# Performance work log

Measured on AMD Instinct MI355X. Metric: run time of the kernel, lower is better.

## Reference

```python
import jax, jax.numpy as jnp
import numpy as np

B, T, D, H = 2, 2048, 768, 12
HS = D // H           # head_size = 64
FF = 4 * D            # feed_forward_multiplier = 4 -> hidden 3072
HALF = FF // 2        # SwiGLU halves hidden -> 1536
EPS = 1e-8


def rmsnorm(x, scale):
    # RMSNorm with p=-1: full-dim L2 norm / sqrt(d), then x/(rms+eps)*scale
    d = x.shape[-1]
    rms = jnp.linalg.norm(x, axis=-1, keepdims=True) * (d ** -0.5)
    return scale * (x / (rms + EPS))


def setup_inputs() -> dict:
    key = jax.random.key(0)
    ks = jax.random.split(key, 12)
    s = 0.02
    return {
        "x":  jax.random.normal(ks[0], (B, T, D), dtype=jnp.float32),
        "Wq": jax.random.normal(ks[1], (H, D, HS), dtype=jnp.float32) * s,
        "Wk": jax.random.normal(ks[2], (H, D, HS), dtype=jnp.float32) * s,
        "Wv": jax.random.normal(ks[3], (H, D, HS), dtype=jnp.float32) * s,
        "Wo": jax.random.normal(ks[4], (D, D), dtype=jnp.float32) * s,
        "bo": jnp.zeros((D,), dtype=jnp.float32),
        "W1": jax.random.normal(ks[5], (D, FF), dtype=jnp.float32) * s,
        "b1": jnp.zeros((FF,), dtype=jnp.float32),
        "W2": jax.random.normal(ks[6], (HALF, D), dtype=jnp.float32) * s,
        "b2": jnp.zeros((D,), dtype=jnp.float32),
        "g1": jnp.ones((D,), dtype=jnp.float32),
        "g2": jnp.ones((D,), dtype=jnp.float32),
    }


def reference(x, Wq, Wk, Wv, Wo, bo, W1, b1, W2, b2, g1, g2):
    Bx, Tx, Dx = x.shape
    # --- Multi-head causal attention (pre-RMSNorm, residual) ---
    h = rmsnorm(x, g1)
    q = jnp.einsum('btd,hdk->bhtk', h, Wq)
    k = jnp.einsum('btd,hdk->bhtk', h, Wk)
    v = jnp.einsum('btd,hdk->bhtk', h, Wv)
    # NOTE: original scales by C**-0.5 where C = embed_dim (not head_size)
    scores = jnp.einsum('bhtk,bhsk->bhts', q, k) * (Dx ** -0.5)
    causal = jnp.tril(jnp.ones((Tx, Tx), dtype=bool))
    scores = jnp.where(causal, scores, -jnp.inf)
    wei = jax.nn.softmax(scores, axis=-1)
    attn = jnp.einsum('bhts,bhsk->bhtk', wei, v)
    attn = attn.transpose(0, 2, 1, 3).reshape(Bx, Tx, Dx)  # concat heads
    x = x + attn @ Wo + bo
    # --- SwiGLU FFN (pre-RMSNorm, residual) ---
    h2 = rmsnorm(x, g2)
    u = h2 @ W1 + b1
    a, gate = jnp.split(u, 2, axis=-1)  # chunk: first half = value, second = gate
    x = x + (jax.nn.silu(gate) * a) @ W2 + b2
    return x
```

## Files before the change

### kernel.cpp

```cpp
#include <hip/hip_runtime.h>
#include <math.h>

#define TDIM 2048
#define DDIM 768
#define NH   12
#define NROWS 4096
#define EPSV 1e-8f
#define SCALE 0.03608439182435161f

typedef __bf16 bf16_t;
typedef bf16_t bf16x8 __attribute__((ext_vector_type(8)));
typedef bf16_t bf16x4 __attribute__((ext_vector_type(4)));
typedef float  floatx4 __attribute__((ext_vector_type(4)));

__device__ __forceinline__ void glds16(const bf16_t* g, bf16_t* l) {
    __builtin_amdgcn_global_load_lds(
        (const __attribute__((address_space(1))) void*)g,
        (__attribute__((address_space(3))) void*)l, 16, 0, 0);
}

__global__ __launch_bounds__(256) void pack_all(
    const float* __restrict__ Wq, const float* __restrict__ Wk,
    const float* __restrict__ Wv, const float* __restrict__ Wo,
    const float* __restrict__ W1, const float* __restrict__ W2,
    bf16_t* __restrict__ qkvw, bf16_t* __restrict__ wo,
    bf16_t* __restrict__ w1, bf16_t* __restrict__ w2)
{
    int bid = blockIdx.x;
    const float* src; bf16_t* dst;
    int srcld, dstld, k0, n0;
    if (bid < 144) {
        int kx = bid % 12, nx = bid / 12;
        src = Wo; dst = wo; srcld = 768; dstld = 768; k0 = kx * 64; n0 = nx * 64;
    } else if (bid < 720) {
        int t = bid - 144; int kx = t % 12, nx = t / 12;
        src = W1; dst = w1; srcld = 3072; dstld = 768; k0 = kx * 64; n0 = nx * 64;
    } else if (bid < 1008) {
        int t = bid - 720; int kx = t % 24, nx = t / 24;
        src = W2; dst = w2; srcld = 768; dstld = 1536; k0 = kx * 64; n0 = nx * 64;
    } else {
        int t = bid - 1008; int kx = t % 12, y = t / 12;
        int sel = y / 12, h = y - sel * 12;
        src = ((sel == 0) ? Wq : (sel == 1) ? Wk : Wv) + (size_t)h * 768 * 64;
        dst = qkvw + (size_t)(sel * 768 + h * 64) * 768;
        srcld = 64; dstld = 768; k0 = kx * 64; n0 = 0;
    }
    __shared__ float Ts[64][65];
    int tid = threadIdx.x;
    int r = tid >> 2, c = (tid & 3) * 16;
    const float* s = src + (size_t)(k0 + r) * srcld + n0 + c;
    #pragma unroll
    for (int i = 0; i < 4; i++) {
        float4 t = *(const float4*)(s + i * 4);
        Ts[r][c + i*4 + 0] = t.x; Ts[r][c + i*4 + 1] = t.y;
        Ts[r][c + i*4 + 2] = t.z; Ts[r][c + i*4 + 3] = t.w;
    }
    __syncthreads();
    int n = tid >> 2, kk = (tid & 3) * 16;
    bf16x8 o0, o1;
    #pragma unroll
    for (int i = 0; i < 8; i++) {
        o0[i] = (bf16_t)Ts[kk + i][n];
        o1[i] = (bf16_t)Ts[kk + 8 + i][n];
    }
    bf16_t* d = dst + (size_t)(n0 + n) * dstld + k0 + kk;
    *(bf16x8*)d = o0;
    *(bf16x8*)(d + 8) = o1;
}

__global__ __launch_bounds__(256) void rmsnorm_bf(
    const float* __restrict__ x, const float* __restrict__ g,
    bf16_t* __restrict__ out)
{
    int row = blockIdx.x;
    int tid = threadIdx.x;
    const float* xr = x + (size_t)row * DDIM;
    float v0 = xr[tid], v1 = xr[tid + 256], v2 = xr[tid + 512];
    float s = v0*v0 + v1*v1 + v2*v2;
    #pragma unroll
    for (int off = 32; off > 0; off >>= 1)
        s += __shfl_down(s, off, 64);
    __shared__ float red[4];
    __shared__ float tot;
    if ((tid & 63) == 0) red[tid >> 6] = s;
    __syncthreads();
    if (tid == 0) tot = red[0] + red[1] + red[2] + red[3];
    __syncthreads();
    float rms = sqrtf(tot * (1.0f / DDIM));
    float inv = 1.0f / (rms + EPSV);
    bf16_t* orow = out + (size_t)row * DDIM;
    orow[tid]       = (bf16_t)(g[tid]       * v0 * inv);
    orow[tid + 256] = (bf16_t)(g[tid + 256] * v1 * inv);
    orow[tid + 512] = (bf16_t)(g[tid + 512] * v2 * inv);
}

template<int TM>
__global__ __launch_bounds__(256) void gemm_bf16(
    const bf16_t* __restrict__ A, const bf16_t* __restrict__ BT, int K,
    float* __restrict__ Cf, bf16_t* __restrict__ Cb, int ldc,
    const float* __restrict__ bias, const float* __restrict__ resid)
{
    constexpr int MT = TM / 32;
    __shared__ bf16_t As0[TM][32], As1[TM][32];
    __shared__ bf16_t Bs0[128][32], Bs1[128][32];
    int tid = threadIdx.x;
    int wave = tid >> 6, lane = tid & 63;
    int lrow = lane & 15, quad = lane >> 4;
    int wm = wave >> 1, wn = wave & 1;

    int m0 = blockIdx.y * TM;
    int n0 = blockIdx.x * 128;

    int srow = lane >> 2, scol = (lane & 3) * 8;
    const bf16_t* Ag = A  + ((size_t)m0 + wave * (TM/4) + srow) * K + scol;
    const bf16_t* Bg = BT + ((size_t)n0 + wave * 32 + srow) * K + scol;

    floatx4 acc[MT][4];
    #pragma unroll
    for (int mt = 0; mt < MT; mt++)
        #pragma unroll
        for (int nt = 0; nt < 4; nt++)
            #pragma unroll
            for (int r = 0; r < 4; r++) acc[mt][nt][r] = 0.f;

    for (int k0 = 0; k0 < K; k0 += 64) {
        __syncthreads();
        #pragma unroll
        for (int i = 0; i < TM/64; i++) {
            glds16(Ag + (size_t)(i*16) * K + k0,      &As0[wave*(TM/4) + i*16][0]);
            glds16(Ag + (size_t)(i*16) * K + k0 + 32, &As1[wave*(TM/4) + i*16][0]);
        }
        #pragma unroll
        for (int i = 0; i < 2; i++) {
            glds16(Bg + (size_t)(i*16) * K + k0,      &Bs0[wave*32 + i*16][0]);
            glds16(Bg + (size_t)(i*16) * K + k0 + 32, &Bs1[wave*32 + i*16][0]);
        }
        __syncthreads();

        bf16x8 af0[MT], af1[MT], bf0[4], bf1[4];
        #pragma unroll
        for (int mt = 0; mt < MT; mt++) {
            af0[mt] = *(const bf16x8*)&As0[wm*(TM/2) + mt*16 + lrow][quad * 8];
            af1[mt] = *(const bf16x8*)&As1[wm*(TM/2) + mt*16 + lrow][quad * 8];
        }
        #pragma unroll
        for (int nt = 0; nt < 4; nt++) {
            bf0[nt] = *(const bf16x8*)&Bs0[wn*64 + nt*16 + lrow][quad * 8];
            bf1[nt] = *(const bf16x8*)&Bs1[wn*64 + nt*16 + lrow][quad * 8];
        }
        #pragma unroll
        for (int mt = 0; mt < MT; mt++)
            #pragma unroll
            for (int nt = 0; nt < 4; nt++) {
                acc[mt][nt] = __builtin_amdgcn_mfma_f32_16x16x32_bf16(
                    bf0[nt], af0[mt], acc[mt][nt], 0, 0, 0);
                acc[mt][nt] = __builtin_amdgcn_mfma_f32_16x16x32_bf16(
                    bf1[nt], af1[mt], acc[mt][nt], 0, 0, 0);
            }
    }

    int crow0 = m0 + wm * (TM/2);
    int ccol0 = n0 + wn * 64;
    #pragma unroll
    for (int mt = 0; mt < MT; mt++) {
        int row = crow0 + mt * 16 + lrow;
        #pragma unroll
        for (int nt = 0; nt < 4; nt++) {
            int col = ccol0 + nt * 16 + quad * 4;
            size_t off = (size_t)row * ldc + col;
            float4 bv = make_float4(0.f, 0.f, 0.f, 0.f);
            if (bias) bv = *(const float4*)(bias + col);
            float4 rs = make_float4(0.f, 0.f, 0.f, 0.f);
            if (resid) rs = *(const float4*)(resid + off);
            floatx4 a = acc[mt][nt];
            if (Cf) {
                float4 v;
                v.x = a[0] + bv.x + rs.x; v.y = a[1] + bv.y + rs.y;
                v.z = a[2] + bv.z + rs.z; v.w = a[3] + bv.w + rs.w;
                *(float4*)(Cf + off) = v;
            } else {
                bf16x4 v;
                v[0] = (bf16_t)(a[0] + bv.x + rs.x);
                v[1] = (bf16_t)(a[1] + bv.y + rs.y);
                v[2] = (bf16_t)(a[2] + bv.z + rs.z);
                v[3] = (bf16_t)(a[3] + bv.w + rs.w);
                *(bf16x4*)(Cb + off) = v;
            }
        }
    }
}

__global__ __launch_bounds__(256) void vt_kernel(
    const bf16_t* __restrict__ qkv, bf16_t* __restrict__ vt)
{
    __shared__ bf16_t Ts[64][72];
    int t0 = blockIdx.x * 64;
    int bh = blockIdx.y;
    int b = bh / NH, h = bh - b * NH;
    int tid = threadIdx.x;
    int r = tid >> 2, c = (tid & 3) * 16;
    const bf16_t* src = qkv + ((size_t)b * TDIM + t0 + r) * 2304 + 1536 + h * 64 + c;
    *(bf16x8*)&Ts[r][c]     = *(const bf16x8*)src;
    *(bf16x8*)&Ts[r][c + 8] = *(const bf16x8*)(src + 8);
    __syncthreads();
    int d = tid >> 2, tt = (tid & 3) * 16;
    bf16x8 o0, o1;
    #pragma unroll
    for (int i = 0; i < 8; i++) {
        o0[i] = Ts[tt + i][d];
        o1[i] = Ts[tt + 8 + i][d];
    }
    bf16_t* dst = vt + ((size_t)bh * 64 + d) * TDIM + t0 + tt;
    *(bf16x8*)dst = o0;
    *(bf16x8*)(dst + 8) = o1;
}

__global__ __launch_bounds__(256) void attn_mfma(
    const bf16_t* __restrict__ qkv, const bf16_t* __restrict__ vt,
    bf16_t* __restrict__ o)
{
    const int QS = 2304;
    int bid = blockIdx.x;
    int j = bid & 255, slot = bid >> 8;
    int qt, bh;
    if (slot == 0)      { qt = j & 31;        bh = j >> 5; }
    else if (slot == 1) { qt = 31 - (j & 31); bh = 8 + (j >> 5); }
    else                { qt = j >> 3;        bh = 16 + (j & 7); }
    int b = bh / NH, h = bh - b * NH;
    int tid = threadIdx.x;
    int wave = tid >> 6, lane = tid & 63;
    int lrow = lane & 15, quad = lane >> 4;

    __shared__ bf16_t Ks[64][72];
    __shared__ bf16_t Vt[64][72];
    __shared__ bf16_t Ps[4][16][72];

    size_t rbase = (size_t)b * TDIM;
    int q0 = qt * 64, qrow_w = q0 + wave * 16;

    const bf16_t* qp = qkv + (rbase + qrow_w + lrow) * QS + h * 64;
    bf16x8 qf[2];
    qf[0] = *(const bf16x8*)(qp + quad * 8);
    qf[1] = *(const bf16x8*)(qp + 32 + quad * 8);

    floatx4 o_acc[4];
    #pragma unroll
    for (int mt = 0; mt < 4; mt++)
        #pragma unroll
        for (int r = 0; r < 4; r++) o_acc[mt][r] = 0.f;
    float m_r = -INFINITY, l_r = 0.f;

    int srow = tid >> 2;
    int scol = (tid & 3) * 16;

    for (int s = 0; s <= qt; s++) {
        __syncthreads();
        {
            const bf16_t* kp = qkv + (rbase + s * 64 + srow) * QS + 768 + h * 64 + scol;
            *(bf16x8*)&Ks[srow][scol]     = *(const bf16x8*)kp;
            *(bf16x8*)&Ks[srow][scol + 8] = *(const bf16x8*)(kp + 8);
            const bf16_t* vp = vt + ((size_t)bh * 64 + srow) * TDIM + s * 64 + scol;
            *(bf16x8*)&Vt[srow][scol]     = *(const bf16x8*)vp;
            *(bf16x8*)&Vt[srow][scol + 8] = *(const bf16x8*)(vp + 8);
        }
        __syncthreads();

        floatx4 sfrag[4];
        #pragma unroll
        for (int nt = 0; nt < 4; nt++) {
            floatx4 a;
            #pragma unroll
            for (int r = 0; r < 4; r++) a[r] = 0.f;
            #pragma unroll
            for (int kf = 0; kf < 2; kf++) {
                bf16x8 afr = *(const bf16x8*)&Ks[nt * 16 + lrow][kf * 32 + quad * 8];
                a = __builtin_amdgcn_mfma_f32_16x16x32_bf16(afr, qf[kf], a, 0, 0, 0);
            }
            sfrag[nt] = a;
        }

        if (s == qt) {
            int qg = qrow_w + lrow;
            #pragma unroll
            for (int nt = 0; nt < 4; nt++)
                #pragma unroll
                for (int r = 0; r < 4; r++) {
                    int kc = s * 64 + nt * 16 + quad * 4 + r;
                    sfrag[nt][r] = (kc > qg) ? -INFINITY : sfrag[nt][r] * SCALE;
                }
        } else {
            #pragma unroll
            for (int nt = 0; nt < 4; nt++)
                #pragma unroll
                for (int r = 0; r < 4; r++) sfrag[nt][r] *= SCALE;
        }

        float mx = sfrag[0][0];
        #pragma unroll
        for (int nt = 0; nt < 4; nt++)
            #pragma unroll
            for (int r = 0; r < 4; r++) mx = fmaxf(mx, sfrag[nt][r]);
        mx = fmaxf(mx, __shfl_xor(mx, 16, 64));
        mx = fmaxf(mx, __shfl_xor(mx, 32, 64));
        float mn = fmaxf(m_r, mx);
        float alpha = __expf(m_r - mn);
        m_r = mn;

        float ls = 0.f;
        #pragma unroll
        for (int nt = 0; nt < 4; nt++) {
            bf16x4 pv;
            #pragma unroll
            for (int r = 0; r < 4; r++) {
                float p = __expf(sfrag[nt][r] - mn);
                ls += p;
                pv[r] = (bf16_t)p;
            }
            *(bf16x4*)&Ps[wave][lrow][nt * 16 + quad * 4] = pv;
        }
        ls += __shfl_xor(ls, 16, 64);
        ls += __shfl_xor(ls, 32, 64);
        l_r = l_r * alpha + ls;
        #pragma unroll
        for (int mt = 0; mt < 4; mt++)
            #pragma unroll
            for (int r = 0; r < 4; r++) o_acc[mt][r] *= alpha;

        #pragma unroll
        for (int kf = 0; kf < 2; kf++) {
            bf16x8 pfr = *(const bf16x8*)&Ps[wave][lrow][kf * 32 + quad * 8];
            #pragma unroll
            for (int mt = 0; mt < 4; mt++) {
                bf16x8 vfr = *(const bf16x8*)&Vt[mt * 16 + lrow][kf * 32 + quad * 8];
                o_acc[mt] = __builtin_amdgcn_mfma_f32_16x16x32_bf16(vfr, pfr, o_acc[mt], 0, 0, 0);
            }
        }
    }

    float inv = 1.0f / l_r;
    size_t rb = (rbase + qrow_w + lrow) * DDIM + h * 64;
    #pragma unroll
    for (int mt = 0; mt < 4; mt++) {
        bf16x4 ov;
        #pragma unroll
        for (int r = 0; r < 4; r++) ov[r] = (bf16_t)(o_acc[mt][r] * inv);
        *(bf16x4*)(o + rb + mt * 16 + quad * 4) = ov;
    }
}

__global__ __launch_bounds__(192) void swiglu_bf(
    const bf16_t* __restrict__ u, bf16_t* __restrict__ sw)
{
    int row = blockIdx.x;
    int j0 = threadIdx.x * 8;
    bf16x8 a = *(const bf16x8*)(u + (size_t)row * 3072 + j0);
    bf16x8 g = *(const bf16x8*)(u + (size_t)row * 3072 + 1536 + j0);
    bf16x8 r;
    #pragma unroll
    for (int i = 0; i < 8; i++) {
        float gv = (float)g[i];
        r[i] = (bf16_t)((float)a[i] * (gv / (1.0f + __expf(-gv))));
    }
    *(bf16x8*)(sw + (size_t)row * 1536 + j0) = r;
}

extern "C" void kernel_launch(void* const* d_in, const int* in_sizes, int n_in,
                              void* d_out, int out_size, void* d_ws, size_t ws_size,
                              hipStream_t stream) {
    const float* x  = (const float*)d_in[0];
    const float* Wq = (const float*)d_in[1];
    const float* Wk = (const float*)d_in[2];
    const float* Wv = (const float*)d_in[3];
    const float* Wo = (const float*)d_in[4];
    const float* bo = (const float*)d_in[5];
    const float* W1 = (const float*)d_in[6];
    const float* b1 = (const float*)d_in[7];
    const float* W2 = (const float*)d_in[8];
    const float* b2 = (const float*)d_in[9];
    const float* g1 = (const float*)d_in[10];
    const float* g2 = (const float*)d_in[11];
    float* out = (float*)d_out;
    char* ws = (char*)d_ws;

    bf16_t* qkvw_bt = (bf16_t*)(ws);
    bf16_t* wo_bt   = (bf16_t*)(ws + 3538944);
    bf16_t* w1_bt   = (bf16_t*)(ws + 4718592);
    bf16_t* w2_bt   = (bf16_t*)(ws + 9437184);
    bf16_t* h_bf    = (bf16_t*)(ws + 11796480);
    bf16_t* qkv     = (bf16_t*)(ws + 18087936);
    bf16_t* attn_bf = (bf16_t*)(ws + 36962304);
    bf16_t* u_bf    = (bf16_t*)(ws + 43253760);
    bf16_t* sw_bf   = (bf16_t*)(ws + 68419584);
    bf16_t* vt      = (bf16_t*)(ws + 81002496);

    pack_all<<<1440, 256, 0, stream>>>(Wq, Wk, Wv, Wo, W1, W2,
                                       qkvw_bt, wo_bt, w1_bt, w2_bt);

    rmsnorm_bf<<<NROWS, 256, 0, stream>>>(x, g1, h_bf);

    gemm_bf16<128><<<dim3(18, 32), 256, 0, stream>>>(
        h_bf, qkvw_bt, 768, nullptr, qkv, 2304, nullptr, nullptr);

    vt_kernel<<<dim3(32, 24), 256, 0, stream>>>(qkv, vt);

    attn_mfma<<<768, 256, 0, stream>>>(qkv, vt, attn_bf);

    gemm_bf16<64><<<dim3(6, 64), 256, 0, stream>>>(
        attn_bf, wo_bt, 768, out, nullptr, 768, bo, x);

    rmsnorm_bf<<<NROWS, 256, 0, stream>>>(out, g2, h_bf);

    gemm_bf16<128><<<dim3(24, 32), 256, 0, stream>>>(
        h_bf, w1_bt, 768, nullptr, u_bf, 3072, b1, nullptr);

    swiglu_bf<<<NROWS, 192, 0, stream>>>(u_bf, sw_bf);

    gemm_bf16<64><<<dim3(6, 64), 256, 0, stream>>>(
        sw_bf, w2_bt, 1536, out, nullptr, 768, b2, out);
}
```

Measured before the change: 269.1 us.

## Fuse SwiGLU into W1 GEMM epilogue and double-buffer attention K/V tiles

Interleaves the value and gate columns of W1 during packing so that each GEMM lane holds matching value/gate pairs. SwiGLU can then be applied in the W1 GEMM epilogue, which removes the separate swiglu kernel and the round trip of the 3072-wide intermediate through memory. The attention kernel now double-buffers K/V tiles in LDS with register prefetch two tiles ahead, cutting one barrier per iteration. It also raises wave priority around the MFMAs and skips the online-softmax rescale unless the running max grows by more than a threshold. The lazy rescale lets exponentials reach up to e^8 before renormalising, and the interleaved bf16x2 stores are narrower than before.

```diff
diff --git a/kernel.cpp b/kernel.cpp
--- a/kernel.cpp
+++ b/kernel.cpp
@@ -11,6 +11,7 @@
 typedef __bf16 bf16_t;
 typedef bf16_t bf16x8 __attribute__((ext_vector_type(8)));
 typedef bf16_t bf16x4 __attribute__((ext_vector_type(4)));
+typedef bf16_t bf16x2 __attribute__((ext_vector_type(2)));
 typedef float  floatx4 __attribute__((ext_vector_type(4)));
 
 __device__ __forceinline__ void glds16(const bf16_t* g, bf16_t* l) {
@@ -29,12 +30,14 @@
     int bid = blockIdx.x;
     const float* src; bf16_t* dst;
     int srcld, dstld, k0, n0;
+    int remap = 0;
     if (bid < 144) {
         int kx = bid % 12, nx = bid / 12;
         src = Wo; dst = wo; srcld = 768; dstld = 768; k0 = kx * 64; n0 = nx * 64;
     } else if (bid < 720) {
         int t = bid - 144; int kx = t % 12, nx = t / 12;
         src = W1; dst = w1; srcld = 3072; dstld = 768; k0 = kx * 64; n0 = nx * 64;
+        remap = 1;
     } else if (bid < 1008) {
         int t = bid - 720; int kx = t % 24, nx = t / 24;
         src = W2; dst = w2; srcld = 768; dstld = 1536; k0 = kx * 64; n0 = nx * 64;
@@ -63,7 +66,9 @@
         o0[i] = (bf16_t)Ts[kk + i][n];
         o1[i] = (bf16_t)Ts[kk + 8 + i][n];
     }
-    bf16_t* d = dst + (size_t)(n0 + n) * dstld + k0 + kk;
+    int oc = n0 + n;
+    if (remap) oc = (oc < 1536) ? (oc * 2) : ((oc - 1536) * 2 + 1);
+    bf16_t* d = dst + (size_t)oc * dstld + k0 + kk;
     *(bf16x8*)d = o0;
     *(bf16x8*)(d + 8) = o1;
 }
@@ -94,7 +99,7 @@
     orow[tid + 512] = (bf16_t)(g[tid + 512] * v2 * inv);
 }
 
-template<int TM>
+template<int TM, int EPI>
 __global__ __launch_bounds__(256) void gemm_bf16(
     const bf16_t* __restrict__ A, const bf16_t* __restrict__ BT, int K,
     float* __restrict__ Cf, bf16_t* __restrict__ Cb, int ldc,
@@ -167,24 +172,36 @@
         #pragma unroll
         for (int nt = 0; nt < 4; nt++) {
             int col = ccol0 + nt * 16 + quad * 4;
-            size_t off = (size_t)row * ldc + col;
-            float4 bv = make_float4(0.f, 0.f, 0.f, 0.f);
-            if (bias) bv = *(const float4*)(bias + col);
-            float4 rs = make_float4(0.f, 0.f, 0.f, 0.f);
-            if (resid) rs = *(const float4*)(resid + off);
             floatx4 a = acc[mt][nt];
-            if (Cf) {
-                float4 v;
-                v.x = a[0] + bv.x + rs.x; v.y = a[1] + bv.y + rs.y;
-                v.z = a[2] + bv.z + rs.z; v.w = a[3] + bv.w + rs.w;
-                *(float4*)(Cf + off) = v;
+            if constexpr (EPI == 1) {
+                int c = col >> 1;
+                float2 ba = *(const float2*)(bias + c);
+                float2 bg = *(const float2*)(bias + 1536 + c);
+                float a0 = a[0] + ba.x, g0 = a[1] + bg.x;
+                float a1 = a[2] + ba.y, g1 = a[3] + bg.y;
+                bf16x2 v;
+                v[0] = (bf16_t)(a0 * (g0 / (1.0f + __expf(-g0))));
+                v[1] = (bf16_t)(a1 * (g1 / (1.0f + __expf(-g1))));
+                *(bf16x2*)(Cb + (size_t)row * ldc + c) = v;
             } else {
-                bf16x4 v;
-                v[0] = (bf16_t)(a[0] + bv.x + rs.x);
-                v[1] = (bf16_t)(a[1] + bv.y + rs.y);
-                v[2] = (bf16_t)(a[2] + bv.z + rs.z);
-                v[3] = (bf16_t)(a[3] + bv.w + rs.w);
-                *(bf16x4*)(Cb + off) = v;
+                size_t off = (size_t)row * ldc + col;
+                float4 bv = make_float4(0.f, 0.f, 0.f, 0.f);
+                if (bias) bv = *(const float4*)(bias + col);
+                float4 rs = make_float4(0.f, 0.f, 0.f, 0.f);
+                if (resid) rs = *(const float4*)(resid + off);
+                if (Cf) {
+                    float4 v;
+                    v.x = a[0] + bv.x + rs.x; v.y = a[1] + bv.y + rs.y;
+                    v.z = a[2] + bv.z + rs.z; v.w = a[3] + bv.w + rs.w;
+                    *(float4*)(Cf + off) = v;
+                } else {
+                    bf16x4 v;
+                    v[0] = (bf16_t)(a[0] + bv.x + rs.x);
+                    v[1] = (bf16_t)(a[1] + bv.y + rs.y);
+                    v[2] = (bf16_t)(a[2] + bv.z + rs.z);
+                    v[3] = (bf16_t)(a[3] + bv.w + rs.w);
+                    *(bf16x4*)(Cb + off) = v;
+                }
             }
         }
     }
@@ -231,8 +248,8 @@
     int wave = tid >> 6, lane = tid & 63;
     int lrow = lane & 15, quad = lane >> 4;
 
-    __shared__ bf16_t Ks[64][72];
-    __shared__ bf16_t Vt[64][72];
+    __shared__ bf16_t Ks[2][64][72];
+    __shared__ bf16_t Vts[2][64][72];
     __shared__ bf16_t Ps[4][16][72];
 
     size_t rbase = (size_t)b * TDIM;
@@ -252,20 +269,31 @@
 
     int srow = tid >> 2;
     int scol = (tid & 3) * 16;
+    const bf16_t* kbase = qkv + (rbase + srow) * QS + 768 + h * 64 + scol;
+    const bf16_t* vbase = vt + ((size_t)bh * 64 + srow) * TDIM + scol;
+
+    bf16x8 kr0 = *(const bf16x8*)kbase;
+    bf16x8 kr1 = *(const bf16x8*)(kbase + 8);
+    bf16x8 vr0 = *(const bf16x8*)vbase;
+    bf16x8 vr1 = *(const bf16x8*)(vbase + 8);
+    *(bf16x8*)&Ks[0][srow][scol]      = kr0;
+    *(bf16x8*)&Ks[0][srow][scol + 8]  = kr1;
+    *(bf16x8*)&Vts[0][srow][scol]     = vr0;
+    *(bf16x8*)&Vts[0][srow][scol + 8] = vr1;
+    if (qt >= 1) {
+        const bf16_t* kp = kbase + (size_t)64 * QS;
+        const bf16_t* vp = vbase + 64;
+        kr0 = *(const bf16x8*)kp;  kr1 = *(const bf16x8*)(kp + 8);
+        vr0 = *(const bf16x8*)vp;  vr1 = *(const bf16x8*)(vp + 8);
+    }
+    asm volatile("s_waitcnt lgkmcnt(0)" ::: "memory");
+    __builtin_amdgcn_s_barrier();
 
     for (int s = 0; s <= qt; s++) {
-        __syncthreads();
-        {
-            const bf16_t* kp = qkv + (rbase + s * 64 + srow) * QS + 768 + h * 64 + scol;
-            *(bf16x8*)&Ks[srow][scol]     = *(const bf16x8*)kp;
-            *(bf16x8*)&Ks[srow][scol + 8] = *(const bf16x8*)(kp + 8);
-            const bf16_t* vp = vt + ((size_t)bh * 64 + srow) * TDIM + s * 64 + scol;
-            *(bf16x8*)&Vt[srow][scol]     = *(const bf16x8*)vp;
-            *(bf16x8*)&Vt[srow][scol + 8] = *(const bf16x8*)(vp + 8);
-        }
-        __syncthreads();
+        int cur = s & 1;
 
         floatx4 sfrag[4];
+        __builtin_amdgcn_s_setprio(1);
         #pragma unroll
         for (int nt = 0; nt < 4; nt++) {
             floatx4 a;
@@ -273,10 +301,19 @@
             for (int r = 0; r < 4; r++) a[r] = 0.f;
             #pragma unroll
             for (int kf = 0; kf < 2; kf++) {
-                bf16x8 afr = *(const bf16x8*)&Ks[nt * 16 + lrow][kf * 32 + quad * 8];
+                bf16x8 afr = *(const bf16x8*)&Ks[cur][nt * 16 + lrow][kf * 32 + quad * 8];
                 a = __builtin_amdgcn_mfma_f32_16x16x32_bf16(afr, qf[kf], a, 0, 0, 0);
             }
             sfrag[nt] = a;
+        }
+        __builtin_amdgcn_s_setprio(0);
+
+        if (s < qt) {
+            int nxt = cur ^ 1;
+            *(bf16x8*)&Ks[nxt][srow][scol]      = kr0;
+            *(bf16x8*)&Ks[nxt][srow][scol + 8]  = kr1;
+            *(bf16x8*)&Vts[nxt][srow][scol]     = vr0;
+            *(bf16x8*)&Vts[nxt][srow][scol + 8] = vr1;
         }
 
         if (s == qt) {
@@ -302,9 +339,16 @@
             for (int r = 0; r < 4; r++) mx = fmaxf(mx, sfrag[nt][r]);
         mx = fmaxf(mx, __shfl_xor(mx, 16, 64));
         mx = fmaxf(mx, __shfl_xor(mx, 32, 64));
-        float mn = fmaxf(m_r, mx);
-        float alpha = __expf(m_r - mn);
-        m_r = mn;
+        if (__any(mx > m_r + 8.0f)) {
+            float mn = fmaxf(m_r, mx);
+            float alpha = __expf(m_r - mn);
+            m_r = mn;
+            l_r *= alpha;
+            #pragma unroll
+            for (int mt = 0; mt < 4; mt++)
+                #pragma unroll
+                for (int r = 0; r < 4; r++) o_acc[mt][r] *= alpha;
+        }
 
         float ls = 0.f;
         #pragma unroll
@@ -312,7 +356,7 @@
             bf16x4 pv;
             #pragma unroll
             for (int r = 0; r < 4; r++) {
-                float p = __expf(sfrag[nt][r] - mn);
+                float p = __expf(sfrag[nt][r] - m_r);
                 ls += p;
                 pv[r] = (bf16_t)p;
             }
@@ -320,21 +364,29 @@
         }
         ls += __shfl_xor(ls, 16, 64);
         ls += __shfl_xor(ls, 32, 64);
-        l_r = l_r * alpha + ls;
-        #pragma unroll
-        for (int mt = 0; mt < 4; mt++)
-            #pragma unroll
-            for (int r = 0; r < 4; r++) o_acc[mt][r] *= alpha;
-
+        l_r += ls;
+
+        __builtin_amdgcn_s_setprio(1);
         #pragma unroll
         for (int kf = 0; kf < 2; kf++) {
             bf16x8 pfr = *(const bf16x8*)&Ps[wave][lrow][kf * 32 + quad * 8];
             #pragma unroll
             for (int mt = 0; mt < 4; mt++) {
-                bf16x8 vfr = *(const bf16x8*)&Vt[mt * 16 + lrow][kf * 32 + quad * 8];
+                bf16x8 vfr = *(const bf16x8*)&Vts[cur][mt * 16 + lrow][kf * 32 + quad * 8];
                 o_acc[mt] = __builtin_amdgcn_mfma_f32_16x16x32_bf16(vfr, pfr, o_acc[mt], 0, 0, 0);
             }
         }
+        __builtin_amdgcn_s_setprio(0);
+
+        if (s + 2 <= qt) {
+            const bf16_t* kp = kbase + (size_t)(s + 2) * 64 * QS;
+            const bf16_t* vp = vbase + (size_t)(s + 2) * 64;
+            kr0 = *(const bf16x8*)kp;  kr1 = *(const bf16x8*)(kp + 8);
+            vr0 = *(const bf16x8*)vp;  vr1 = *(const bf16x8*)(vp + 8);
+        }
+
+        asm volatile("s_waitcnt lgkmcnt(0)" ::: "memory");
+        __builtin_amdgcn_s_barrier();
     }
 
     float inv = 1.0f / l_r;
@@ -346,22 +398,6 @@
         for (int r = 0; r < 4; r++) ov[r] = (bf16_t)(o_acc[mt][r] * inv);
         *(bf16x4*)(o + rb + mt * 16 + quad * 4) = ov;
     }
-}
-
-__global__ __launch_bounds__(192) void swiglu_bf(
-    const bf16_t* __restrict__ u, bf16_t* __restrict__ sw)
-{
-    int row = blockIdx.x;
-    int j0 = threadIdx.x * 8;
-    bf16x8 a = *(const bf16x8*)(u + (size_t)row * 3072 + j0);
-    bf16x8 g = *(const bf16x8*)(u + (size_t)row * 3072 + 1536 + j0);
-    bf16x8 r;
-    #pragma unroll
-    for (int i = 0; i < 8; i++) {
-        float gv = (float)g[i];
-        r[i] = (bf16_t)((float)a[i] * (gv / (1.0f + __expf(-gv))));
-    }
-    *(bf16x8*)(sw + (size_t)row * 1536 + j0) = r;
 }
 
 extern "C" void kernel_launch(void* const* d_in, const int* in_sizes, int n_in,
@@ -389,7 +425,6 @@
     bf16_t* h_bf    = (bf16_t*)(ws + 11796480);
     bf16_t* qkv     = (bf16_t*)(ws + 18087936);
     bf16_t* attn_bf = (bf16_t*)(ws + 36962304);
-    bf16_t* u_bf    = (bf16_t*)(ws + 43253760);
     bf16_t* sw_bf   = (bf16_t*)(ws + 68419584);
     bf16_t* vt      = (bf16_t*)(ws + 81002496);
 
@@ -398,23 +433,21 @@
 
     rmsnorm_bf<<<NROWS, 256, 0, stream>>>(x, g1, h_bf);
 
-    gemm_bf16<128><<<dim3(18, 32), 256, 0, stream>>>(
+    gemm_bf16<128, 0><<<dim3(18, 32), 256, 0, stream>>>(
         h_bf, qkvw_bt, 768, nullptr, qkv, 2304, nullptr, nullptr);
 
     vt_kernel<<<dim3(32, 24), 256, 0, stream>>>(qkv, vt);
 
     attn_mfma<<<768, 256, 0, stream>>>(qkv, vt, attn_bf);
 
-    gemm_bf16<64><<<dim3(6, 64), 256, 0, stream>>>(
+    gemm_bf16<64, 0><<<dim3(6, 64), 256, 0, stream>>>(
         attn_bf, wo_bt, 768, out, nullptr, 768, bo, x);
 
     rmsnorm_bf<<<NROWS, 256, 0, stream>>>(out, g2, h_bf);
 
-    gemm_bf16<128><<<dim3(24, 32), 256, 0, stream>>>(
-        h_bf, w1_bt, 768, nullptr, u_bf, 3072, b1, nullptr);
-
-    swiglu_bf<<<NROWS, 192, 0, stream>>>(u_bf, sw_bf);
-
-    gemm_bf16<64><<<dim3(6, 64), 256, 0, stream>>>(
+    gemm_bf16<128, 1><<<dim3(24, 32), 256, 0, stream>>>(
+        h_bf, w1_bt, 768, nullptr, sw_bf, 1536, b1, nullptr);
+
+    gemm_bf16<64, 0><<<dim3(6, 64), 256, 0, stream>>>(
         sw_bf, w2_bt, 1536, out, nullptr, 768, b2, out);
 }
```

Measured after the change: 264.5 us. About the same (-1.7%).
